# Performance work log

Hardware: AMD Instinct MI355X
Metric: run time of the kernel (lower is better)

The kernel has to match this reference:

```python
import jax, jax.numpy as jnp
import numpy as np

D_MODEL = 768
N_HEAD = 12
N_BR = 4
DH = D_MODEL // N_HEAD          # 64
H_TOT = N_BR * N_HEAD           # 48
K_TOP = 4
B, T = 2, 1024


def setup_inputs() -> dict:
    key = jax.random.key(0)
    ks = jax.random.split(key, 16)
    s = 0.02
    return {
        "A": jax.random.normal(ks[0], (B, T, D_MODEL), jnp.float32),
        "X": jax.random.normal(ks[1], (B, T, D_MODEL), jnp.float32),
        "WK_w": jax.random.normal(ks[2], (D_MODEL, D_MODEL), jnp.float32) * s,
        "WK_b": jax.random.normal(ks[3], (D_MODEL,), jnp.float32) * s,
        "WQ_w": jax.random.normal(ks[4], (D_MODEL * N_BR, D_MODEL), jnp.float32) * s,
        "wedge_A": jax.random.normal(ks[5], (DH, DH), jnp.float32) * s,
        "wedge_bias": jax.random.normal(ks[6], (H_TOT, DH), jnp.float32) * s,
        "sink": jax.random.normal(ks[7], (H_TOT,), jnp.float32) * s,
        "v_nulls": jax.random.normal(ks[8], (N_BR, D_MODEL), jnp.float32) * s,
        "V1_w": jax.random.normal(ks[9], (4 * DH, DH), jnp.float32) * s,
        "V1_b": jax.random.normal(ks[10], (4 * DH,), jnp.float32) * s,
        "V2_w": jax.random.normal(ks[11], (DH, 4 * DH), jnp.float32) * s,
        "V2_b": jax.random.normal(ks[12], (DH,), jnp.float32) * s,
        "WO_w": jax.random.normal(ks[13], (N_BR, D_MODEL, D_MODEL), jnp.float32) * s,
        "WO_b": jax.random.normal(ks[14], (N_BR, D_MODEL), jnp.float32) * s,
    }


def _wedge(x, wedge_A, wedge_bias):
    # S = (A - A^T) + diag_embed(id_bias); x: [B,H,T,Dh]
    skew = wedge_A - wedge_A.T                       # [Dh,Dh]
    S = skew[None, :, :] + jax.vmap(jnp.diag)(wedge_bias)  # [H,Dh,Dh]
    return x + jnp.einsum('bhtd,hde->bhte', x, S)


def _rope(x):
    # x: [B,H,T,Dh]; halves are interleaved-split then concatenated
    t_len = x.shape[2]
    inv_freq = 1.0 / (10000.0 ** (jnp.arange(0, DH, 2, dtype=jnp.float32) / DH))
    freqs = jnp.arange(t_len, dtype=jnp.float32)[:, None] * inv_freq[None, :]  # [T,Dh/2]
    cos = jnp.cos(freqs)[None, None]
    sin = jnp.sin(freqs)[None, None]
    x1 = x[..., 0::2]
    x2 = x[..., 1::2]
    return jnp.concatenate((-x2 * sin + x1 * cos, x1 * sin + x2 * cos), axis=-1)


def reference(A, X, WK_w, WK_b, WQ_w, wedge_A, wedge_bias, sink, v_nulls,
              V1_w, V1_b, V2_w, V2_b, WO_w, WO_b):
    b, t, c = A.shape
    scale = DH ** -0.5

    q = (A @ WQ_w.T).reshape(b, t, H_TOT, DH).transpose(0, 2, 1, 3)     # [B,Htot,T,Dh]
    k_base = X @ WK_w.T + WK_b
    k = k_base.reshape(b, t, N_HEAD, DH).transpose(0, 2, 1, 3)          # [B,Nsh,T,Dh]
    k = jnp.tile(k, (1, N_BR, 1, 1))                                    # [B,Htot,T,Dh]

    q = _rope(_wedge(q, wedge_A, wedge_bias))
    k = _rope(_wedge(k, wedge_A, wedge_bias))

    scores = jnp.einsum('bhtd,bhsd->bhts', q, k) * scale                # [B,Htot,T,T]
    causal = jnp.triu(jnp.ones((t, t), dtype=bool), k=1)
    scores = jnp.where(causal[None, None], -jnp.inf, scores)

    sinks = jnp.broadcast_to(sink.reshape(1, H_TOT, 1, 1), (b, H_TOT, t, 1))
    probs_full = jax.nn.softmax(jnp.concatenate([scores, sinks], axis=-1), axis=-1)
    probs_tokens = probs_full[..., :t]
    probs_sink = probs_full[..., t:]                                    # [B,Htot,T,1]

    k_top = min(K_TOP, t)
    vals, idxs = jax.lax.top_k(probs_tokens, k_top)                     # [B,Htot,T,K]
    weights = vals / (jnp.sum(vals, axis=-1, keepdims=True) + 1e-9)

    # gather top-k keys: [B,Htot,T,K,Dh]
    k_selected = jnp.take_along_axis(k[:, :, None, :, :], idxs[..., None], axis=3)
    marker = jnp.einsum('bhtk,bhtkd->bhtd', weights, k_selected)        # [B,Htot,T,Dh]

    h = jax.nn.gelu(marker @ V1_w.T + V1_b, approximate=False)
    out_tokens = h @ V2_w.T + V2_b                                      # [B,Htot,T,Dh]

    v_null = v_nulls.reshape(H_TOT, DH)[None, :, None, :]
    context = out_tokens + probs_sink * v_null                          # [B,Htot,T,Dh]

    context = context.reshape(b, N_BR, N_HEAD, t, DH)
    context = context.transpose(0, 1, 3, 2, 4).reshape(b, N_BR, t, c)   # [B,Nbr,T,C]

    y = jnp.einsum('bntc,ncd->bntd', context, WO_w) + WO_b[None, :, None, :]
    return y.mean(axis=1)
```

## Files before the change

kernel.cpp:

```cpp
#include <hip/hip_runtime.h>
#include <math.h>

constexpr int Bq  = 2;
constexpr int Tq  = 1024;
constexpr int HTq = 48;
constexpr float SCALE = 0.125f;

typedef __attribute__((ext_vector_type(8))) short short8;
typedef __attribute__((ext_vector_type(4))) float f32x4;

__device__ inline unsigned short f2bf(float x) {
    unsigned u = __float_as_uint(x);
    return (unsigned short)((u + 0x7FFF + ((u >> 16) & 1)) >> 16);
}

__device__ inline void split3(float x, unsigned short& p0, unsigned short& p1, unsigned short& p2) {
    p0 = f2bf(x);
    float f0 = __uint_as_float((unsigned)p0 << 16);
    float r0 = x - f0;
    p1 = f2bf(r0);
    float f1 = __uint_as_float((unsigned)p1 << 16);
    float r1 = r0 - f1;
    p2 = f2bf(r1);
}

__device__ inline float gelu_f(float x) {
    float z = 0.70710678118654752f * x;
    float az = fabsf(z);
    float t = __frcp_rn(1.0f + 0.3275911f * az);
    float poly = t * (0.254829592f + t * (-0.284496736f + t * (1.421413741f
               + t * (-1.453152027f + t * 1.061405429f))));
    float er = 1.0f - poly * __expf(-az * az);
    er = (z < 0.0f) ? -er : er;
    return 0.5f * x * (1.0f + er);
}

__global__ void trig_kernel(float* __restrict__ trig) {
    int i = blockIdx.x * 256 + threadIdx.x;
    int t = i >> 5, f = i & 31;
    float invf = powf(10000.0f, -(float)f * (1.0f / 32.0f));
    float ang = (float)t * invf;
    trig[i] = cosf(ang);
    trig[32768 + i] = sinf(ang);
}

__global__ __launch_bounds__(256) void fold_split_kernel(
    const float* __restrict__ Wsrc, const float* __restrict__ wA,
    const float* __restrict__ wbias, unsigned short* __restrict__ Wsp, int mode)
{
    const size_t WPL = (size_t)4608 * 768;
    __shared__ float sw[64][132];
    __shared__ float sk[64][65];
    int h = blockIdx.x, cb = blockIdx.y;
    int tid = threadIdx.x;
    const float* Wh = Wsrc + (size_t)h * 64 * 768 + cb * 128;
    for (int l = tid; l < 64 * 32; l += 256) {
        int d = l >> 5, c4 = l & 31;
        *(float4*)&sw[d][c4 * 4] = *(const float4*)(Wh + (size_t)d * 768 + c4 * 4);
    }
    for (int l = tid; l < 4096; l += 256) {
        int d = l >> 6, e = l & 63;
        sk[d][e] = wA[l] - wA[e * 64 + d];
    }
    __syncthreads();
    int tx = tid & 15, ty = tid >> 4;
    float acc4[4][8] = {};
    for (int d = 0; d < 64; d++) {
        float s0 = sk[d][ty * 4 + 0], s1 = sk[d][ty * 4 + 1];
        float s2 = sk[d][ty * 4 + 2], s3 = sk[d][ty * 4 + 3];
        float w_[8];
        *(float4*)&w_[0] = *(const float4*)&sw[d][tx * 8];
        *(float4*)&w_[4] = *(const float4*)&sw[d][tx * 8 + 4];
        #pragma unroll
        for (int j = 0; j < 8; j++) {
            acc4[0][j] += s0 * w_[j];
            acc4[1][j] += s1 * w_[j];
            acc4[2][j] += s2 * w_[j];
            acc4[3][j] += s3 * w_[j];
        }
    }
    #pragma unroll
    for (int i = 0; i < 4; i++) {
        int e = ty * 4 + i;
        float scale = (mode == 0) ? (1.0f + wbias[h * 64 + e]) : 1.0f;
        size_t row = (mode == 0) ? (size_t)(h * 64 + e) : (size_t)(3072 + h * 64 + e);
        #pragma unroll
        for (int j = 0; j < 8; j++) {
            int cl = tx * 8 + j;
            float wv = sw[e][cl] * scale + acc4[i][j];
            unsigned short p0, p1, p2;
            split3(wv, p0, p1, p2);
            size_t idx = row * 768 + cb * 128 + cl;
            Wsp[idx] = p0; Wsp[WPL + idx] = p1; Wsp[2 * WPL + idx] = p2;
        }
        if (mode == 1) {
            size_t row2 = (size_t)(3840 + h * 64 + e);
            #pragma unroll
            for (int j = 0; j < 8; j++) {
                int cl = tx * 8 + j;
                unsigned short p0, p1, p2;
                split3(sw[e][cl], p0, p1, p2);
                size_t idx = row2 * 768 + cb * 128 + cl;
                Wsp[idx] = p0; Wsp[WPL + idx] = p1; Wsp[2 * WPL + idx] = p2;
            }
        }
    }
}

__global__ void kbias_kernel(const float* __restrict__ WKb, const float* __restrict__ wA,
                             float* __restrict__ bcat) {
    int e = blockIdx.x * 256 + threadIdx.x;
    if (e < 768) {
        int hb = e >> 6, el = e & 63;
        float acc = 0.0f;
        for (int d = 0; d < 64; d++) {
            float sk = wA[d * 64 + el] - wA[el * 64 + d];
            acc += WKb[hb * 64 + d] * sk;
        }
        bcat[e] = WKb[e] + acc;
    } else if (e < 1536) {
        bcat[e] = WKb[e - 768];
    }
}

__global__ void split_act_kernel(const float* __restrict__ A, const float* __restrict__ X,
                                 unsigned short* __restrict__ Asp, unsigned short* __restrict__ Xsp)
{
    const size_t APL = (size_t)2048 * 768;
    int i = blockIdx.x * 256 + threadIdx.x;
    if (i >= 393216) return;
    float4 va = ((const float4*)A)[i];
    float4 vx = ((const float4*)X)[i];
    ushort4 a0, a1, a2, x0, x1, x2;
    split3(va.x, a0.x, a1.x, a2.x); split3(va.y, a0.y, a1.y, a2.y);
    split3(va.z, a0.z, a1.z, a2.z); split3(va.w, a0.w, a1.w, a2.w);
    split3(vx.x, x0.x, x1.x, x2.x); split3(vx.y, x0.y, x1.y, x2.y);
    split3(vx.z, x0.z, x1.z, x2.z); split3(vx.w, x0.w, x1.w, x2.w);
    ((ushort4*)(Asp))[i] = a0;
    ((ushort4*)(Asp + APL))[i] = a1;
    ((ushort4*)(Asp + 2 * APL))[i] = a2;
    ((ushort4*)(Xsp))[i] = x0;
    ((ushort4*)(Xsp + APL))[i] = x1;
    ((ushort4*)(Xsp + 2 * APL))[i] = x2;
}

__global__ __launch_bounds__(512) void proj_mfma_kernel(
    const unsigned short* __restrict__ Asp, const unsigned short* __restrict__ Xsp,
    const unsigned short* __restrict__ Wsp, const float* __restrict__ bcat,
    const float* __restrict__ trig, float* __restrict__ Qr, float* __restrict__ O2)
{
    const size_t APL = (size_t)2048 * 768;
    const size_t WPL = (size_t)4608 * 768;
    __shared__ unsigned short sA[3 * 128 * 40];
    __shared__ unsigned short sB[3 * 128 * 40];
    int bid = blockIdx.x;
    int swz = (bid & 7) * 72 + (bid >> 3);
    int nb = swz >> 4;
    int mb = swz & 15;
    bool isQ = (nb < 24);
    const unsigned short* Ab = isQ ? Asp : Xsp;
    int m0 = mb * 128, n0 = nb * 128;
    int tid = threadIdx.x;
    int w = tid >> 6, lane = tid & 63;
    int wm = w & 1, wn = w >> 1;
    int rf = lane & 15, kg = lane >> 4;
    int mbase = m0 + wm * 64;

    int sp_[3], sr_[3], ss_[3];
    #pragma unroll
    for (int i = 0; i < 3; i++) {
        int s = tid + i * 512;
        sp_[i] = s >> 9; sr_[i] = (s >> 2) & 127; ss_[i] = s & 3;
    }

    f32x4 acc[4][2] = {};
    for (int k0 = 0; k0 < 768; k0 += 32) {
        __syncthreads();
        #pragma unroll
        for (int i = 0; i < 3; i++) {
            short8 va = *(const short8*)(Ab + (size_t)sp_[i] * APL + (size_t)(m0 + sr_[i]) * 768 + k0 + ss_[i] * 8);
            short8 vb = *(const short8*)(Wsp + (size_t)sp_[i] * WPL + (size_t)(n0 + sr_[i]) * 768 + k0 + ss_[i] * 8);
            *(short8*)&sA[sp_[i] * 5120 + sr_[i] * 40 + ss_[i] * 8] = va;
            *(short8*)&sB[sp_[i] * 5120 + sr_[i] * 40 + ss_[i] * 8] = vb;
        }
        __syncthreads();

        short8 a0[4], a1[4], a2[4], b0[2], b1[2], b2[2];
        #pragma unroll
        for (int mi = 0; mi < 4; mi++) {
            int row = wm * 64 + mi * 16 + rf;
            a0[mi] = *(const short8*)&sA[0 * 5120 + row * 40 + kg * 8];
        }
        #pragma unroll
        for (int nj = 0; nj < 2; nj++) {
            int row = wn * 32 + nj * 16 + rf;
            b0[nj] = *(const short8*)&sB[0 * 5120 + row * 40 + kg * 8];
        }
        #pragma unroll
        for (int mi = 0; mi < 4; mi++)
            #pragma unroll
            for (int nj = 0; nj < 2; nj++)
                acc[mi][nj] = __builtin_amdgcn_mfma_f32_16x16x32_bf16(a0[mi], b0[nj], acc[mi][nj], 0, 0, 0);
        #pragma unroll
        for (int nj = 0; nj < 2; nj++) {
            int row = wn * 32 + nj * 16 + rf;
            b1[nj] = *(const short8*)&sB[1 * 5120 + row * 40 + kg * 8];
        }
        #pragma unroll
        for (int mi = 0; mi < 4; mi++)
            #pragma unroll
            for (int nj = 0; nj < 2; nj++)
                acc[mi][nj] = __builtin_amdgcn_mfma_f32_16x16x32_bf16(a0[mi], b1[nj], acc[mi][nj], 0, 0, 0);
        #pragma unroll
        for (int nj = 0; nj < 2; nj++) {
            int row = wn * 32 + nj * 16 + rf;
            b2[nj] = *(const short8*)&sB[2 * 5120 + row * 40 + kg * 8];
        }
        #pragma unroll
        for (int mi = 0; mi < 4; mi++)
            #pragma unroll
            for (int nj = 0; nj < 2; nj++)
                acc[mi][nj] = __builtin_amdgcn_mfma_f32_16x16x32_bf16(a0[mi], b2[nj], acc[mi][nj], 0, 0, 0);
        #pragma unroll
        for (int mi = 0; mi < 4; mi++) {
            int row = wm * 64 + mi * 16 + rf;
            a1[mi] = *(const short8*)&sA[1 * 5120 + row * 40 + kg * 8];
        }
        #pragma unroll
        for (int mi = 0; mi < 4; mi++)
            #pragma unroll
            for (int nj = 0; nj < 2; nj++)
                acc[mi][nj] = __builtin_amdgcn_mfma_f32_16x16x32_bf16(a1[mi], b0[nj], acc[mi][nj], 0, 0, 0);
        #pragma unroll
        for (int mi = 0; mi < 4; mi++)
            #pragma unroll
            for (int nj = 0; nj < 2; nj++)
                acc[mi][nj] = __builtin_amdgcn_mfma_f32_16x16x32_bf16(a1[mi], b1[nj], acc[mi][nj], 0, 0, 0);
        #pragma unroll
        for (int mi = 0; mi < 4; mi++) {
            int row = wm * 64 + mi * 16 + rf;
            a2[mi] = *(const short8*)&sA[2 * 5120 + row * 40 + kg * 8];
        }
        #pragma unroll
        for (int mi = 0; mi < 4; mi++)
            #pragma unroll
            for (int nj = 0; nj < 2; nj++)
                acc[mi][nj] = __builtin_amdgcn_mfma_f32_16x16x32_bf16(a2[mi], b0[nj], acc[mi][nj], 0, 0, 0);
    }

    if (isQ) {
        #pragma unroll
        for (int mi = 0; mi < 4; mi++) {
            #pragma unroll
            for (int r = 0; r < 4; r++) {
                int m = mbase + mi * 16 + kg * 4 + r;
                int b_ = m >> 10, t = m & 1023;
                #pragma unroll
                for (int nj = 0; nj < 2; nj++) {
                    int col_local = wn * 32 + nj * 16 + rf;
                    int h = nb * 2 + (col_local >> 6);
                    int d = col_local & 63;
                    int i = d >> 1;
                    float v = acc[mi][nj][r];
                    float pv = __shfl_xor(v, 1);
                    float c = trig[t * 32 + i];
                    float s = trig[32768 + t * 32 + i];
                    float outv = (rf & 1) ? (pv * s + v * c) : (v * c - pv * s);
                    int col = (rf & 1) ? (32 + i) : i;
                    size_t base = ((size_t)(b_ * 48 + h) * 1024 + t) * 64;
                    Qr[base + col] = outv;
                }
            }
        }
    } else {
        #pragma unroll
        for (int nj = 0; nj < 2; nj++) {
            int col = (n0 - 3072) + wn * 32 + nj * 16 + rf;
            float bv = bcat[col];
            #pragma unroll
            for (int mi = 0; mi < 4; mi++)
                #pragma unroll
                for (int r = 0; r < 4; r++) {
                    int m = mbase + mi * 16 + kg * 4 + r;
                    O2[(size_t)m * 1536 + col] = acc[mi][nj][r] + bv;
                }
        }
    }
}

__global__ void k_finish_kernel(const float* __restrict__ O2, const float* __restrict__ trig,
                                const float* __restrict__ wbias,
                                float* __restrict__ Kr, unsigned short* __restrict__ Kb16)
{
    int idx = blockIdx.x * 256 + threadIdx.x;
    int pr = idx & 31;
    int tmp = idx >> 5;
    int hb = tmp % 12;
    int bt = tmp / 12;
    int t = bt & 1023, b = bt >> 10;
    const float* yx = O2 + (size_t)bt * 1536 + hb * 64 + pr * 2;
    float y0 = yx[0], y1 = yx[1];
    float x0 = yx[768], x1 = yx[769];
    float cv = trig[t * 32 + pr], sv = trig[32768 + t * 32 + pr];
    #pragma unroll
    for (int r = 0; r < 4; r++) {
        int h = hb + 12 * r;
        float b0 = wbias[h * 64 + 2 * pr], b1 = wbias[h * 64 + 2 * pr + 1];
        float wz0 = y0 + x0 * b0;
        float wz1 = y1 + x1 * b1;
        float lo = wz0 * cv - wz1 * sv;
        float hi = wz0 * sv + wz1 * cv;
        size_t base = ((size_t)(b * 48 + h) * 1024 + t) * 64;
        Kr[base + pr] = lo;
        Kr[base + 32 + pr] = hi;
        Kb16[base + pr] = f2bf(lo);
        Kb16[base + 32 + pr] = f2bf(hi);
    }
}

__global__ __launch_bounds__(256) void attn_mfma_topk_kernel(
    const float* __restrict__ Qr, const float* __restrict__ Kr,
    const unsigned short* __restrict__ Kb, const float* __restrict__ sink,
    unsigned short* __restrict__ markerb, float* __restrict__ psink)
{
    const int bh = blockIdx.x;
    const int qb = 15 - (int)blockIdx.y;
    const int w = threadIdx.x >> 6, lane = threadIdx.x & 63;
    const int rf = lane & 15, kg = lane >> 4;
    const int h = bh % HTq;
    const int q0 = qb * 64 + w * 16;
    const size_t rowbase = (size_t)bh * Tq;

    short8 a0, a1;
    {
        const float* qp = Qr + (rowbase + q0 + rf) * 64 + kg * 8;
        float4 u0 = *(const float4*)qp;
        float4 u1 = *(const float4*)(qp + 4);
        float4 u2 = *(const float4*)(qp + 32);
        float4 u3 = *(const float4*)(qp + 36);
        a0[0]=(short)f2bf(u0.x); a0[1]=(short)f2bf(u0.y); a0[2]=(short)f2bf(u0.z); a0[3]=(short)f2bf(u0.w);
        a0[4]=(short)f2bf(u1.x); a0[5]=(short)f2bf(u1.y); a0[6]=(short)f2bf(u1.z); a0[7]=(short)f2bf(u1.w);
        a1[0]=(short)f2bf(u2.x); a1[1]=(short)f2bf(u2.y); a1[2]=(short)f2bf(u2.z); a1[3]=(short)f2bf(u2.w);
        a1[4]=(short)f2bf(u3.x); a1[5]=(short)f2bf(u3.y); a1[6]=(short)f2bf(u3.z); a1[7]=(short)f2bf(u3.w);
    }

    float m_[4], Z_[4], tv[4][4];
    int ti[4][4];
    #pragma unroll
    for (int r = 0; r < 4; r++) {
        m_[r] = -1e30f; Z_[r] = 0.0f;
        #pragma unroll
        for (int p = 0; p < 4; p++) { tv[r][p] = -INFINITY; ti[r][p] = -1; }
    }

    const int T = (q0 + 15) / 64 + 1;
    const unsigned short* Kbb = Kb + rowbase * 64;
    for (int tile = 0; tile < T; tile++) {
        const int s0 = tile << 6;
        f32x4 accs[4];
        #pragma unroll
        for (int kc = 0; kc < 4; kc++) {
            const unsigned short* kp = Kbb + (size_t)(s0 + kc * 16 + rf) * 64 + kg * 8;
            short8 b0 = *(const short8*)kp;
            short8 b1 = *(const short8*)(kp + 32);
            f32x4 acc = {0.f, 0.f, 0.f, 0.f};
            acc = __builtin_amdgcn_mfma_f32_16x16x32_bf16(a0, b0, acc, 0, 0, 0);
            acc = __builtin_amdgcn_mfma_f32_16x16x32_bf16(a1, b1, acc, 0, 0, 0);
            accs[kc] = acc;
        }
        const bool lastt = (tile == T - 1);
        #pragma unroll
        for (int r = 0; r < 4; r++) {
            const int trow = q0 + kg * 4 + r;
            float sv[4];
            #pragma unroll
            for (int kc = 0; kc < 4; kc++) {
                int k = s0 + kc * 16 + rf;
                float s = accs[kc][r] * SCALE;
                sv[kc] = (lastt && k > trow) ? -INFINITY : s;
            }
            float tm = fmaxf(fmaxf(sv[0], sv[1]), fmaxf(sv[2], sv[3]));
            float nm = fmaxf(m_[r], tm);
            float zz = Z_[r] * __expf(m_[r] - nm);
            #pragma unroll
            for (int kc = 0; kc < 4; kc++) zz += __expf(sv[kc] - nm);
            Z_[r] = zz; m_[r] = nm;
            #pragma unroll
            for (int kc = 0; kc < 4; kc++) {
                float v = sv[kc]; int id = s0 + kc * 16 + rf;
                #pragma unroll
                for (int p = 0; p < 4; p++) {
                    bool sw = v > tv[r][p];
                    float ov = tv[r][p]; int oi = ti[r][p];
                    tv[r][p] = sw ? v : ov;  ti[r][p] = sw ? id : oi;
                    v = sw ? ov : v;          id = sw ? oi : id;
                }
            }
        }
    }

    const float sk = sink[h];
    #pragma unroll 1
    for (int r = 0; r < 4; r++) {
        const int q = q0 + kg * 4 + r;
        float m = m_[r], Z = Z_[r];
        #pragma unroll
        for (int off = 1; off < 16; off <<= 1) {
            float om = __shfl_xor(m, off);
            float oz = __shfl_xor(Z, off);
            float nm = fmaxf(m, om);
            Z = Z * __expf(m - nm) + oz * __expf(om - nm);
            m = nm;
        }
        float av[4]; int ai[4];
        #pragma unroll
        for (int p = 0; p < 4; p++) { av[p] = tv[r][p]; ai[p] = ti[r][p]; }
        float cvv[8]; int ci[8];
        #pragma unroll
        for (int rd = 0; rd < 8; rd++) {
            float v = av[0]; int id = ai[0];
            #pragma unroll
            for (int off = 1; off < 16; off <<= 1) {
                float ov = __shfl_xor(v, off);
                int oi = __shfl_xor(id, off);
                bool take = (ov > v) || ((ov == v) && ((unsigned)oi < (unsigned)id));
                v = take ? ov : v; id = take ? oi : id;
            }
            cvv[rd] = v; ci[rd] = id;
            bool own = (ai[0] == id) && (av[0] == v);
            av[0] = own ? av[1] : av[0];  ai[0] = own ? ai[1] : ai[0];
            av[1] = own ? av[2] : av[1];  ai[1] = own ? ai[2] : ai[1];
            av[2] = own ? av[3] : av[2];  ai[2] = own ? ai[3] : ai[2];
            av[3] = own ? -INFINITY : av[3]; ai[3] = own ? -1 : ai[3];
        }
        const float4 qv = *(const float4*)(Qr + (rowbase + q) * 64 + rf * 4);
        float sc[8];
        #pragma unroll
        for (int c = 0; c < 8; c++) {
            int idx = ci[c] < 0 ? 0 : ci[c];
            const float4 kv = *(const float4*)(Kr + (rowbase + idx) * 64 + rf * 4);
            float p = qv.x * kv.x + qv.y * kv.y + qv.z * kv.z + qv.w * kv.w;
            #pragma unroll
            for (int off = 1; off < 16; off <<= 1) p += __shfl_xor(p, off);
            sc[c] = (ci[c] < 0) ? -1e30f : p * SCALE;
        }
        float bv[4]; int bi[4];
        #pragma unroll
        for (int rd = 0; rd < 4; rd++) {
            float v = sc[0]; int id = ci[0];
            #pragma unroll
            for (int c = 1; c < 8; c++) {
                bool take = (sc[c] > v) || ((sc[c] == v) && ((unsigned)ci[c] < (unsigned)id));
                v = take ? sc[c] : v; id = take ? ci[c] : id;
            }
            bv[rd] = v; bi[rd] = id;
            #pragma unroll
            for (int c = 0; c < 8; c++) {
                bool kill = (ci[c] == id) && (sc[c] == v);
                sc[c] = kill ? -3e30f : sc[c];
            }
        }
        float mf = fmaxf(m, sk);
        float Zf = Z * __expf(m - mf) + __expf(sk - mf);
        float e0 = __expf(bv[0] - mf), e1 = __expf(bv[1] - mf);
        float e2 = __expf(bv[2] - mf), e3 = __expf(bv[3] - mf);
        float wsum = e0 + e1 + e2 + e3 + Zf * 1e-9f;
        float w0 = e0 / wsum, w1 = e1 / wsum, w2 = e2 / wsum, w3 = e3 / wsum;
        int i0 = bi[0] < 0 ? 0 : bi[0];
        int i1 = bi[1] < 0 ? 0 : bi[1];
        int i2 = bi[2] < 0 ? 0 : bi[2];
        int i3 = bi[3] < 0 ? 0 : bi[3];
        const float4 k0 = *(const float4*)(Kr + (rowbase + i0) * 64 + rf * 4);
        const float4 k1 = *(const float4*)(Kr + (rowbase + i1) * 64 + rf * 4);
        const float4 k2 = *(const float4*)(Kr + (rowbase + i2) * 64 + rf * 4);
        const float4 k3 = *(const float4*)(Kr + (rowbase + i3) * 64 + rf * 4);
        float mx = w0 * k0.x + w1 * k1.x + w2 * k2.x + w3 * k3.x;
        float my = w0 * k0.y + w1 * k1.y + w2 * k2.y + w3 * k3.y;
        float mz = w0 * k0.z + w1 * k1.z + w2 * k2.z + w3 * k3.z;
        float mw = w0 * k0.w + w1 * k1.w + w2 * k2.w + w3 * k3.w;
        ushort4 mo;
        mo.x = f2bf(mx); mo.y = f2bf(my); mo.z = f2bf(mz); mo.w = f2bf(mw);
        *(ushort4*)(markerb + (rowbase + q) * 64 + rf * 4) = mo;
        if (rf == 0) psink[rowbase + q] = __expf(sk - mf) / Zf;
    }
}

__global__ void cvt_bf16_kernel(const float* __restrict__ in,
                                unsigned short* __restrict__ out, int n4)
{
    int i = blockIdx.x * 256 + threadIdx.x;
    if (i < n4) {
        float4 v = ((const float4*)in)[i];
        ushort4 o;
        o.x = f2bf(v.x); o.y = f2bf(v.y); o.z = f2bf(v.z); o.w = f2bf(v.w);
        ((ushort4*)out)[i] = o;
    }
}

__global__ __launch_bounds__(256) void wo_transpose_kernel(
    const float* __restrict__ WOw, unsigned short* __restrict__ WOt)
{
    __shared__ float tl[64][65];
    int tid = threadIdx.x;
    int n = blockIdx.z;
    int c0 = blockIdx.x * 64, d0 = blockIdx.y * 64;
    const float* src = WOw + (size_t)n * 768 * 768;
    for (int l = tid; l < 64 * 16; l += 256) {
        int r = l >> 4, q = l & 15;
        float4 v = *(const float4*)(src + (size_t)(c0 + r) * 768 + d0 + q * 4);
        tl[r][q * 4 + 0] = v.x; tl[r][q * 4 + 1] = v.y;
        tl[r][q * 4 + 2] = v.z; tl[r][q * 4 + 3] = v.w;
    }
    __syncthreads();
    for (int l = tid; l < 64 * 16; l += 256) {
        int d = l >> 4, q = l & 15;
        ushort4 o;
        o.x = f2bf(tl[q * 4 + 0][d]); o.y = f2bf(tl[q * 4 + 1][d]);
        o.z = f2bf(tl[q * 4 + 2][d]); o.w = f2bf(tl[q * 4 + 3][d]);
        *(ushort4*)(WOt + (size_t)n * 768 * 768 + (size_t)(d0 + d) * 768 + c0 + q * 4) = o;
    }
}

__global__ __launch_bounds__(256) void mlp_mfma_kernel(
    const unsigned short* __restrict__ markerb, const float* __restrict__ psink,
    const unsigned short* __restrict__ V1b16, const float* __restrict__ V1bias,
    const unsigned short* __restrict__ V2b16, const float* __restrict__ V2bias,
    const float* __restrict__ vnulls, unsigned short* __restrict__ ctxb)
{
    __shared__ float h_lds[4][16][65];
    int tid = threadIdx.x;
    int w = tid >> 6, lane = tid & 63;
    int rf = lane & 15, kg = lane >> 4;
    size_t r0 = (size_t)blockIdx.x * 64 + 16 * w;

    short8 a1[2];
    #pragma unroll
    for (int kk = 0; kk < 2; kk++)
        a1[kk] = *(const short8*)(markerb + (r0 + rf) * 64 + kk * 32 + kg * 8);

    f32x4 acc2[4] = {};
    for (int ch = 0; ch < 4; ch++) {
        f32x4 acc1[4] = {};
        #pragma unroll
        for (int nj = 0; nj < 4; nj++)
            #pragma unroll
            for (int kk = 0; kk < 2; kk++) {
                short8 b1 = *(const short8*)(V1b16 + (size_t)(ch * 64 + nj * 16 + rf) * 64 + kk * 32 + kg * 8);
                acc1[nj] = __builtin_amdgcn_mfma_f32_16x16x32_bf16(a1[kk], b1, acc1[nj], 0, 0, 0);
            }
        __syncthreads();
        #pragma unroll
        for (int nj = 0; nj < 4; nj++) {
            float bb = V1bias[ch * 64 + nj * 16 + rf];
            #pragma unroll
            for (int r = 0; r < 4; r++) {
                float x = acc1[nj][r] + bb;
                h_lds[w][kg * 4 + r][nj * 16 + rf] = gelu_f(x);
            }
        }
        __syncthreads();
        #pragma unroll
        for (int kk = 0; kk < 2; kk++) {
            const float* hp = &h_lds[w][rf][kk * 32 + kg * 8];
            float4 p0 = *(const float4*)hp;
            float4 p1 = *(const float4*)(hp + 4);
            short8 a2;
            a2[0] = (short)f2bf(p0.x); a2[1] = (short)f2bf(p0.y);
            a2[2] = (short)f2bf(p0.z); a2[3] = (short)f2bf(p0.w);
            a2[4] = (short)f2bf(p1.x); a2[5] = (short)f2bf(p1.y);
            a2[6] = (short)f2bf(p1.z); a2[7] = (short)f2bf(p1.w);
            #pragma unroll
            for (int njo = 0; njo < 4; njo++) {
                short8 b2 = *(const short8*)(V2b16 + (size_t)(njo * 16 + rf) * 256 + ch * 64 + kk * 32 + kg * 8);
                acc2[njo] = __builtin_amdgcn_mfma_f32_16x16x32_bf16(a2, b2, acc2[njo], 0, 0, 0);
            }
        }
    }
    #pragma unroll
    for (int r = 0; r < 4; r++) {
        size_t R = r0 + kg * 4 + r;
        int bh = (int)(R >> 10), t = (int)(R & 1023);
        int b = bh / 48, h = bh % 48;
        int n = h / 12, head = h % 12;
        float ps = psink[R];
        size_t base = ((size_t)((b * 4 + n) * 1024 + t)) * 768 + head * 64;
        #pragma unroll
        for (int njo = 0; njo < 4; njo++) {
            int d = njo * 16 + rf;
            float v = acc2[njo][r] + V2bias[d] + ps * vnulls[h * 64 + d];
            ctxb[base + d] = f2bf(v);
        }
    }
}

__global__ __launch_bounds__(256) void gemm_wo_mfma(
    const unsigned short* __restrict__ ctxb, const unsigned short* __restrict__ WOtb,
    const float* __restrict__ WOb, float* __restrict__ Out)
{
    __shared__ unsigned short sA[64 * 64];
    __shared__ unsigned short sB[64 * 64];
    int tid = threadIdx.x;
    int w = tid >> 6, lane = tid & 63;
    int wm = w >> 1, wn = w & 1;
    int rf = lane & 15, kg = lane >> 4;
    int m0 = blockIdx.x * 64, n0 = blockIdx.y * 64;
    int b = m0 >> 10, t0 = m0 & 1023;
    int c0 = tid * 2, c1 = tid * 2 + 1;
    int ra = c0 >> 3, ca = c0 & 7, rb = c1 >> 3, cb = c1 & 7;
    f32x4 acc[2][2] = {};
    for (int n = 0; n < 4; n++) {
        const unsigned short* Ab = ctxb + ((size_t)((b * 4 + n) * 1024 + t0)) * 768;
        const unsigned short* Bb = WOtb + (size_t)n * 768 * 768 + (size_t)n0 * 768;
        for (int k0 = 0; k0 < 768; k0 += 64) {
            __syncthreads();
            *(short8*)&sA[ra * 64 + ((ca ^ (ra & 7)) * 8)] = *(const short8*)(Ab + (size_t)ra * 768 + k0 + ca * 8);
            *(short8*)&sA[rb * 64 + ((cb ^ (rb & 7)) * 8)] = *(const short8*)(Ab + (size_t)rb * 768 + k0 + cb * 8);
            *(short8*)&sB[ra * 64 + ((ca ^ (ra & 7)) * 8)] = *(const short8*)(Bb + (size_t)ra * 768 + k0 + ca * 8);
            *(short8*)&sB[rb * 64 + ((cb ^ (rb & 7)) * 8)] = *(const short8*)(Bb + (size_t)rb * 768 + k0 + cb * 8);
            __syncthreads();
            #pragma unroll
            for (int kk = 0; kk < 2; kk++) {
                int kc = kk * 4 + kg;
                int rA0 = wm * 32 + rf, rA1 = wm * 32 + 16 + rf;
                int rB0 = wn * 32 + rf, rB1 = wn * 32 + 16 + rf;
                short8 a0v = *(const short8*)&sA[rA0 * 64 + ((kc ^ (rA0 & 7)) * 8)];
                short8 a1v = *(const short8*)&sA[rA1 * 64 + ((kc ^ (rA1 & 7)) * 8)];
                short8 b0v = *(const short8*)&sB[rB0 * 64 + ((kc ^ (rB0 & 7)) * 8)];
                short8 b1v = *(const short8*)&sB[rB1 * 64 + ((kc ^ (rB1 & 7)) * 8)];
                acc[0][0] = __builtin_amdgcn_mfma_f32_16x16x32_bf16(a0v, b0v, acc[0][0], 0, 0, 0);
                acc[0][1] = __builtin_amdgcn_mfma_f32_16x16x32_bf16(a0v, b1v, acc[0][1], 0, 0, 0);
                acc[1][0] = __builtin_amdgcn_mfma_f32_16x16x32_bf16(a1v, b0v, acc[1][0], 0, 0, 0);
                acc[1][1] = __builtin_amdgcn_mfma_f32_16x16x32_bf16(a1v, b1v, acc[1][1], 0, 0, 0);
            }
        }
    }
    #pragma unroll
    for (int nj = 0; nj < 2; nj++) {
        int col = n0 + wn * 32 + nj * 16 + rf;
        float bm = WOb[col] + WOb[768 + col] + WOb[1536 + col] + WOb[2304 + col];
        #pragma unroll
        for (int mi = 0; mi < 2; mi++)
            #pragma unroll
            for (int r = 0; r < 4; r++) {
                int row = m0 + wm * 32 + mi * 16 + kg * 4 + r;
                Out[(size_t)row * 768 + col] = 0.25f * (acc[mi][nj][r] + bm);
            }
    }
}

extern "C" void kernel_launch(void* const* d_in, const int* in_sizes, int n_in,
                              void* d_out, int out_size, void* d_ws, size_t ws_size,
                              hipStream_t stream) {
    const float* A      = (const float*)d_in[0];
    const float* X      = (const float*)d_in[1];
    const float* WKw    = (const float*)d_in[2];
    const float* WKb    = (const float*)d_in[3];
    const float* WQw    = (const float*)d_in[4];
    const float* wA     = (const float*)d_in[5];
    const float* wB     = (const float*)d_in[6];
    const float* sink   = (const float*)d_in[7];
    const float* vnulls = (const float*)d_in[8];
    const float* V1w    = (const float*)d_in[9];
    const float* V1b    = (const float*)d_in[10];
    const float* V2w    = (const float*)d_in[11];
    const float* V2b    = (const float*)d_in[12];
    const float* WOw    = (const float*)d_in[13];
    const float* WOb    = (const float*)d_in[14];
    float* out = (float*)d_out;
    (void)in_sizes; (void)n_in; (void)out_size; (void)ws_size;

    float* ws = (float*)d_ws;
    size_t off = 0;
    float* Qr   = ws + off;  off += 6291456;
    float* Kr   = ws + off;  off += 6291456;
    float* trig = ws + off;  off += 65536;
    float* bcat = ws + off;  off += 2048;
    float* O2   = ws + off;  off += 3145728;
    float* Wsp_f = ws + off; off += 5308416;
    unsigned short* Wsp = (unsigned short*)Wsp_f;
    unsigned short* Asp = (unsigned short*)(ws + off); off += 2359296;
    unsigned short* Xsp = (unsigned short*)(ws + off); off += 2359296;
    unsigned short* markerb = (unsigned short*)O2;
    unsigned short* Kb16 = Wsp;
    float* psink = Wsp_f + 3145728;
    unsigned short* V1b16 = Xsp;
    unsigned short* V2b16 = V1b16 + 16384;
    unsigned short* WOtb  = Asp;
    unsigned short* ctxb  = (unsigned short*)Qr;

    trig_kernel<<<128, 256, 0, stream>>>(trig);
    fold_split_kernel<<<dim3(48, 6), 256, 0, stream>>>(WQw, wA, wB, Wsp, 0);
    fold_split_kernel<<<dim3(12, 6), 256, 0, stream>>>(WKw, wA, wB, Wsp, 1);
    kbias_kernel<<<6, 256, 0, stream>>>(WKb, wA, bcat);
    split_act_kernel<<<1536, 256, 0, stream>>>(A, X, Asp, Xsp);
    proj_mfma_kernel<<<576, 512, 0, stream>>>(Asp, Xsp, Wsp, bcat, trig, Qr, O2);
    k_finish_kernel<<<3072, 256, 0, stream>>>(O2, trig, wB, Kr, Kb16);
    attn_mfma_topk_kernel<<<dim3(96, 16), 256, 0, stream>>>(Qr, Kr, Kb16, sink, markerb, psink);
    cvt_bf16_kernel<<<16, 256, 0, stream>>>(V1w, V1b16, 4096);
    cvt_bf16_kernel<<<16, 256, 0, stream>>>(V2w, V2b16, 4096);
    wo_transpose_kernel<<<dim3(12, 12, 4), 256, 0, stream>>>(WOw, WOtb);
    mlp_mfma_kernel<<<1536, 256, 0, stream>>>(markerb, psink, V1b16, V1b, V2b16, V2b, vnulls, ctxb);
    gemm_wo_mfma<<<dim3(32, 12), 256, 0, stream>>>(ctxb, WOtb, WOb, out);
}
```

Before: 362.7 us.

## Pair causal query blocks, prefetch K tiles, and pack top-k keys into uints

Each attention block now handles two query blocks (qb and 15-qb) so every block does the same amount of causal work, and the grid is halved. The K tile loop is double-buffered in registers so the next tile's loads are issued before the current tile's softmax and top-k work, and the causal mask is applied only on the final diagonal tile. The per-lane top-4 now holds one packed unsigned key (order-preserving score bits with the index in the low 10 bits), which makes the insertion and cross-lane reductions cheaper. Dropping the low mantissa bits can change candidate order on near-ties, but candidates are rescored exactly in fp32 afterwards; the extra prefetch buffers raise register pressure.

```diff
diff --git a/kernel.cpp b/kernel.cpp
--- a/kernel.cpp
+++ b/kernel.cpp
@@ -324,164 +324,228 @@
     unsigned short* __restrict__ markerb, float* __restrict__ psink)
 {
     const int bh = blockIdx.x;
-    const int qb = 15 - (int)blockIdx.y;
+    const int y  = blockIdx.y;
     const int w = threadIdx.x >> 6, lane = threadIdx.x & 63;
     const int rf = lane & 15, kg = lane >> 4;
     const int h = bh % HTq;
-    const int q0 = qb * 64 + w * 16;
     const size_t rowbase = (size_t)bh * Tq;
-
-    short8 a0, a1;
-    {
-        const float* qp = Qr + (rowbase + q0 + rf) * 64 + kg * 8;
-        float4 u0 = *(const float4*)qp;
-        float4 u1 = *(const float4*)(qp + 4);
-        float4 u2 = *(const float4*)(qp + 32);
-        float4 u3 = *(const float4*)(qp + 36);
-        a0[0]=(short)f2bf(u0.x); a0[1]=(short)f2bf(u0.y); a0[2]=(short)f2bf(u0.z); a0[3]=(short)f2bf(u0.w);
-        a0[4]=(short)f2bf(u1.x); a0[5]=(short)f2bf(u1.y); a0[6]=(short)f2bf(u1.z); a0[7]=(short)f2bf(u1.w);
-        a1[0]=(short)f2bf(u2.x); a1[1]=(short)f2bf(u2.y); a1[2]=(short)f2bf(u2.z); a1[3]=(short)f2bf(u2.w);
-        a1[4]=(short)f2bf(u3.x); a1[5]=(short)f2bf(u3.y); a1[6]=(short)f2bf(u3.z); a1[7]=(short)f2bf(u3.w);
-    }
-
-    float m_[4], Z_[4], tv[4][4];
-    int ti[4][4];
-    #pragma unroll
-    for (int r = 0; r < 4; r++) {
-        m_[r] = -1e30f; Z_[r] = 0.0f;
-        #pragma unroll
-        for (int p = 0; p < 4; p++) { tv[r][p] = -INFINITY; ti[r][p] = -1; }
-    }
-
-    const int T = (q0 + 15) / 64 + 1;
     const unsigned short* Kbb = Kb + rowbase * 64;
-    for (int tile = 0; tile < T; tile++) {
-        const int s0 = tile << 6;
-        f32x4 accs[4];
-        #pragma unroll
-        for (int kc = 0; kc < 4; kc++) {
-            const unsigned short* kp = Kbb + (size_t)(s0 + kc * 16 + rf) * 64 + kg * 8;
-            short8 b0 = *(const short8*)kp;
-            short8 b1 = *(const short8*)(kp + 32);
-            f32x4 acc = {0.f, 0.f, 0.f, 0.f};
-            acc = __builtin_amdgcn_mfma_f32_16x16x32_bf16(a0, b0, acc, 0, 0, 0);
-            acc = __builtin_amdgcn_mfma_f32_16x16x32_bf16(a1, b1, acc, 0, 0, 0);
-            accs[kc] = acc;
-        }
-        const bool lastt = (tile == T - 1);
+    const float sk = sink[h];
+
+    #pragma unroll 1
+    for (int g = 0; g < 2; g++) {
+        const int qb = g ? y : 15 - y;
+        const int q0 = qb * 64 + w * 16;
+
+        short8 a0, a1;
+        {
+            const float* qp = Qr + (rowbase + q0 + rf) * 64 + kg * 8;
+            float4 u0 = *(const float4*)qp;
+            float4 u1 = *(const float4*)(qp + 4);
+            float4 u2 = *(const float4*)(qp + 32);
+            float4 u3 = *(const float4*)(qp + 36);
+            a0[0]=(short)f2bf(u0.x); a0[1]=(short)f2bf(u0.y); a0[2]=(short)f2bf(u0.z); a0[3]=(short)f2bf(u0.w);
+            a0[4]=(short)f2bf(u1.x); a0[5]=(short)f2bf(u1.y); a0[6]=(short)f2bf(u1.z); a0[7]=(short)f2bf(u1.w);
+            a1[0]=(short)f2bf(u2.x); a1[1]=(short)f2bf(u2.y); a1[2]=(short)f2bf(u2.z); a1[3]=(short)f2bf(u2.w);
+            a1[4]=(short)f2bf(u3.x); a1[5]=(short)f2bf(u3.y); a1[6]=(short)f2bf(u3.z); a1[7]=(short)f2bf(u3.w);
+        }
+
+        float m_[4], Z_[4];
+        unsigned t_[4][4];
         #pragma unroll
         for (int r = 0; r < 4; r++) {
-            const int trow = q0 + kg * 4 + r;
-            float sv[4];
+            m_[r] = -1e30f; Z_[r] = 0.0f;
+            t_[r][0] = 0u; t_[r][1] = 0u; t_[r][2] = 0u; t_[r][3] = 0u;
+        }
+
+        short8 cA0[4], cA1[4], cB0[4], cB1[4];
+        {
+            const unsigned short* p = Kbb + (size_t)rf * 64 + kg * 8;
             #pragma unroll
             for (int kc = 0; kc < 4; kc++) {
-                int k = s0 + kc * 16 + rf;
-                float s = accs[kc][r] * SCALE;
-                sv[kc] = (lastt && k > trow) ? -INFINITY : s;
-            }
-            float tm = fmaxf(fmaxf(sv[0], sv[1]), fmaxf(sv[2], sv[3]));
-            float nm = fmaxf(m_[r], tm);
-            float zz = Z_[r] * __expf(m_[r] - nm);
-            #pragma unroll
-            for (int kc = 0; kc < 4; kc++) zz += __expf(sv[kc] - nm);
-            Z_[r] = zz; m_[r] = nm;
+                cA0[kc] = *(const short8*)(p + kc * 1024);
+                cA1[kc] = *(const short8*)(p + kc * 1024 + 32);
+            }
+        }
+
+        auto body = [&](short8 (&cb0)[4], short8 (&cb1)[4],
+                        short8 (&nb0)[4], short8 (&nb1)[4], int tile) {
+            f32x4 accs[4];
             #pragma unroll
             for (int kc = 0; kc < 4; kc++) {
-                float v = sv[kc]; int id = s0 + kc * 16 + rf;
-                #pragma unroll
-                for (int p = 0; p < 4; p++) {
-                    bool sw = v > tv[r][p];
-                    float ov = tv[r][p]; int oi = ti[r][p];
-                    tv[r][p] = sw ? v : ov;  ti[r][p] = sw ? id : oi;
-                    v = sw ? ov : v;          id = sw ? oi : id;
+                f32x4 acc = {0.f, 0.f, 0.f, 0.f};
+                acc = __builtin_amdgcn_mfma_f32_16x16x32_bf16(a0, cb0[kc], acc, 0, 0, 0);
+                acc = __builtin_amdgcn_mfma_f32_16x16x32_bf16(a1, cb1[kc], acc, 0, 0, 0);
+                accs[kc] = acc;
+            }
+            const unsigned short* np = Kbb + (size_t)((tile + 1) * 64 + rf) * 64 + kg * 8;
+            #pragma unroll
+            for (int kc = 0; kc < 4; kc++) {
+                nb0[kc] = *(const short8*)(np + kc * 1024);
+                nb1[kc] = *(const short8*)(np + kc * 1024 + 32);
+            }
+            const int s0 = tile << 6;
+            #pragma unroll
+            for (int r = 0; r < 4; r++) {
+                float sv[4];
+                #pragma unroll
+                for (int kc = 0; kc < 4; kc++) sv[kc] = accs[kc][r] * SCALE;
+                #pragma unroll
+                for (int kc = 0; kc < 4; kc++) {
+                    unsigned u = __float_as_uint(sv[kc]);
+                    unsigned key = u ^ ((unsigned)(((int)u) >> 31) | 0x80000000u);
+                    unsigned c = (key & 0xFFFFFC00u) | (unsigned)(s0 + kc * 16 + rf);
+                    unsigned n;
+                    n = t_[r][0] > c ? t_[r][0] : c;  c = t_[r][0] > c ? c : t_[r][0];  t_[r][0] = n;
+                    n = t_[r][1] > c ? t_[r][1] : c;  c = t_[r][1] > c ? c : t_[r][1];  t_[r][1] = n;
+                    n = t_[r][2] > c ? t_[r][2] : c;  c = t_[r][2] > c ? c : t_[r][2];  t_[r][2] = n;
+                    t_[r][3] = t_[r][3] > c ? t_[r][3] : c;
                 }
-            }
-        }
-    }
-
-    const float sk = sink[h];
-    #pragma unroll 1
-    for (int r = 0; r < 4; r++) {
-        const int q = q0 + kg * 4 + r;
-        float m = m_[r], Z = Z_[r];
-        #pragma unroll
-        for (int off = 1; off < 16; off <<= 1) {
-            float om = __shfl_xor(m, off);
-            float oz = __shfl_xor(Z, off);
-            float nm = fmaxf(m, om);
-            Z = Z * __expf(m - nm) + oz * __expf(om - nm);
-            m = nm;
-        }
-        float av[4]; int ai[4];
-        #pragma unroll
-        for (int p = 0; p < 4; p++) { av[p] = tv[r][p]; ai[p] = ti[r][p]; }
-        float cvv[8]; int ci[8];
-        #pragma unroll
-        for (int rd = 0; rd < 8; rd++) {
-            float v = av[0]; int id = ai[0];
+                float tm = fmaxf(fmaxf(sv[0], sv[1]), fmaxf(sv[2], sv[3]));
+                float nm = fmaxf(m_[r], tm);
+                float zz = Z_[r] * __expf(m_[r] - nm);
+                #pragma unroll
+                for (int kc = 0; kc < 4; kc++) zz += __expf(sv[kc] - nm);
+                Z_[r] = zz; m_[r] = nm;
+            }
+        };
+
+        int tile = 0;
+        for (; tile + 1 < qb; tile += 2) {
+            body(cA0, cA1, cB0, cB1, tile);
+            body(cB0, cB1, cA0, cA1, tile + 1);
+        }
+        if (tile < qb) {
+            body(cA0, cA1, cB0, cB1, tile);
+            #pragma unroll
+            for (int kc = 0; kc < 4; kc++) { cA0[kc] = cB0[kc]; cA1[kc] = cB1[kc]; }
+        }
+
+        {
+            f32x4 accs[4];
+            #pragma unroll
+            for (int kc = 0; kc < 4; kc++) {
+                f32x4 acc = {0.f, 0.f, 0.f, 0.f};
+                acc = __builtin_amdgcn_mfma_f32_16x16x32_bf16(a0, cA0[kc], acc, 0, 0, 0);
+                acc = __builtin_amdgcn_mfma_f32_16x16x32_bf16(a1, cA1[kc], acc, 0, 0, 0);
+                accs[kc] = acc;
+            }
+            const int s0 = qb << 6;
+            #pragma unroll
+            for (int r = 0; r < 4; r++) {
+                const int trow = q0 + kg * 4 + r;
+                float sv[4];
+                unsigned pk[4];
+                #pragma unroll
+                for (int kc = 0; kc < 4; kc++) {
+                    int k = s0 + kc * 16 + rf;
+                    bool ok = (k <= trow);
+                    float s = accs[kc][r] * SCALE;
+                    sv[kc] = ok ? s : -INFINITY;
+                    unsigned u = __float_as_uint(s);
+                    unsigned key = u ^ ((unsigned)(((int)u) >> 31) | 0x80000000u);
+                    unsigned c = (key & 0xFFFFFC00u) | (unsigned)k;
+                    pk[kc] = ok ? c : 0u;
+                }
+                #pragma unroll
+                for (int kc = 0; kc < 4; kc++) {
+                    unsigned c = pk[kc], n;
+                    n = t_[r][0] > c ? t_[r][0] : c;  c = t_[r][0] > c ? c : t_[r][0];  t_[r][0] = n;
+                    n = t_[r][1] > c ? t_[r][1] : c;  c = t_[r][1] > c ? c : t_[r][1];  t_[r][1] = n;
+                    n = t_[r][2] > c ? t_[r][2] : c;  c = t_[r][2] > c ? c : t_[r][2];  t_[r][2] = n;
+                    t_[r][3] = t_[r][3] > c ? t_[r][3] : c;
+                }
+                float tm = fmaxf(fmaxf(sv[0], sv[1]), fmaxf(sv[2], sv[3]));
+                float nm = fmaxf(m_[r], tm);
+                float zz = Z_[r] * __expf(m_[r] - nm);
+                #pragma unroll
+                for (int kc = 0; kc < 4; kc++) zz += __expf(sv[kc] - nm);
+                Z_[r] = zz; m_[r] = nm;
+            }
+        }
+
+        #pragma unroll 1
+        for (int r = 0; r < 4; r++) {
+            const int q = q0 + kg * 4 + r;
+            float m = m_[r], Z = Z_[r];
             #pragma unroll
             for (int off = 1; off < 16; off <<= 1) {
-                float ov = __shfl_xor(v, off);
-                int oi = __shfl_xor(id, off);
-                bool take = (ov > v) || ((ov == v) && ((unsigned)oi < (unsigned)id));
-                v = take ? ov : v; id = take ? oi : id;
-            }
-            cvv[rd] = v; ci[rd] = id;
-            bool own = (ai[0] == id) && (av[0] == v);
-            av[0] = own ? av[1] : av[0];  ai[0] = own ? ai[1] : ai[0];
-            av[1] = own ? av[2] : av[1];  ai[1] = own ? ai[2] : ai[1];
-            av[2] = own ? av[3] : av[2];  ai[2] = own ? ai[3] : ai[2];
-            av[3] = own ? -INFINITY : av[3]; ai[3] = own ? -1 : ai[3];
-        }
-        const float4 qv = *(const float4*)(Qr + (rowbase + q) * 64 + rf * 4);
-        float sc[8];
-        #pragma unroll
-        for (int c = 0; c < 8; c++) {
-            int idx = ci[c] < 0 ? 0 : ci[c];
-            const float4 kv = *(const float4*)(Kr + (rowbase + idx) * 64 + rf * 4);
-            float p = qv.x * kv.x + qv.y * kv.y + qv.z * kv.z + qv.w * kv.w;
-            #pragma unroll
-            for (int off = 1; off < 16; off <<= 1) p += __shfl_xor(p, off);
-            sc[c] = (ci[c] < 0) ? -1e30f : p * SCALE;
-        }
-        float bv[4]; int bi[4];
-        #pragma unroll
-        for (int rd = 0; rd < 4; rd++) {
-            float v = sc[0]; int id = ci[0];
-            #pragma unroll
-            for (int c = 1; c < 8; c++) {
-                bool take = (sc[c] > v) || ((sc[c] == v) && ((unsigned)ci[c] < (unsigned)id));
-                v = take ? sc[c] : v; id = take ? ci[c] : id;
-            }
-            bv[rd] = v; bi[rd] = id;
+                float om = __shfl_xor(m, off);
+                float oz = __shfl_xor(Z, off);
+                float nm = fmaxf(m, om);
+                Z = Z * __expf(m - nm) + oz * __expf(om - nm);
+                m = nm;
+            }
+            unsigned l0 = t_[r][0], l1 = t_[r][1], l2 = t_[r][2], l3 = t_[r][3];
+            unsigned ck[8];
+            #pragma unroll
+            for (int rd = 0; rd < 8; rd++) {
+                unsigned v = l0;
+                #pragma unroll
+                for (int off = 1; off < 16; off <<= 1) {
+                    unsigned ov = (unsigned)__shfl_xor((int)v, off);
+                    v = v > ov ? v : ov;
+                }
+                ck[rd] = v;
+                bool own = (l0 == v);
+                l0 = own ? l1 : l0;
+                l1 = own ? l2 : l1;
+                l2 = own ? l3 : l2;
+                l3 = own ? 0u : l3;
+            }
+            const float4 qv = *(const float4*)(Qr + (rowbase + q) * 64 + rf * 4);
+            float sc[8]; int ci[8];
             #pragma unroll
             for (int c = 0; c < 8; c++) {
-                bool kill = (ci[c] == id) && (sc[c] == v);
-                sc[c] = kill ? -3e30f : sc[c];
-            }
-        }
-        float mf = fmaxf(m, sk);
-        float Zf = Z * __expf(m - mf) + __expf(sk - mf);
-        float e0 = __expf(bv[0] - mf), e1 = __expf(bv[1] - mf);
-        float e2 = __expf(bv[2] - mf), e3 = __expf(bv[3] - mf);
-        float wsum = e0 + e1 + e2 + e3 + Zf * 1e-9f;
-        float w0 = e0 / wsum, w1 = e1 / wsum, w2 = e2 / wsum, w3 = e3 / wsum;
-        int i0 = bi[0] < 0 ? 0 : bi[0];
-        int i1 = bi[1] < 0 ? 0 : bi[1];
-        int i2 = bi[2] < 0 ? 0 : bi[2];
-        int i3 = bi[3] < 0 ? 0 : bi[3];
-        const float4 k0 = *(const float4*)(Kr + (rowbase + i0) * 64 + rf * 4);
-        const float4 k1 = *(const float4*)(Kr + (rowbase + i1) * 64 + rf * 4);
-        const float4 k2 = *(const float4*)(Kr + (rowbase + i2) * 64 + rf * 4);
-        const float4 k3 = *(const float4*)(Kr + (rowbase + i3) * 64 + rf * 4);
-        float mx = w0 * k0.x + w1 * k1.x + w2 * k2.x + w3 * k3.x;
-        float my = w0 * k0.y + w1 * k1.y + w2 * k2.y + w3 * k3.y;
-        float mz = w0 * k0.z + w1 * k1.z + w2 * k2.z + w3 * k3.z;
-        float mw = w0 * k0.w + w1 * k1.w + w2 * k2.w + w3 * k3.w;
-        ushort4 mo;
-        mo.x = f2bf(mx); mo.y = f2bf(my); mo.z = f2bf(mz); mo.w = f2bf(mw);
-        *(ushort4*)(markerb + (rowbase + q) * 64 + rf * 4) = mo;
-        if (rf == 0) psink[rowbase + q] = __expf(sk - mf) / Zf;
+                bool valid = (ck[c] != 0u);
+                int idx = (int)(ck[c] & 1023u);
+                int lidx = valid ? idx : 0;
+                const float4 kv = *(const float4*)(Kr + (rowbase + lidx) * 64 + rf * 4);
+                float p = qv.x * kv.x + qv.y * kv.y + qv.z * kv.z + qv.w * kv.w;
+                #pragma unroll
+                for (int off = 1; off < 16; off <<= 1) p += __shfl_xor(p, off);
+                sc[c] = valid ? p * SCALE : -1e30f;
+                ci[c] = valid ? idx : -1;
+            }
+            float bv[4]; int bi[4];
+            #pragma unroll
+            for (int rd = 0; rd < 4; rd++) {
+                float v = sc[0]; int id = ci[0];
+                #pragma unroll
+                for (int c = 1; c < 8; c++) {
+                    bool take = (sc[c] > v) || ((sc[c] == v) && ((unsigned)ci[c] < (unsigned)id));
+                    v = take ? sc[c] : v; id = take ? ci[c] : id;
+                }
+                bv[rd] = v; bi[rd] = id;
+                #pragma unroll
+                for (int c = 0; c < 8; c++) {
+                    bool kill = (ci[c] == id) && (sc[c] == v);
+                    sc[c] = kill ? -3e30f : sc[c];
+                }
+            }
+            float mf = fmaxf(m, sk);
+            float Zf = Z * __expf(m - mf) + __expf(sk - mf);
+            float e0 = __expf(bv[0] - mf), e1 = __expf(bv[1] - mf);
+            float e2 = __expf(bv[2] - mf), e3 = __expf(bv[3] - mf);
+            float wsum = e0 + e1 + e2 + e3 + Zf * 1e-9f;
+            float w0 = e0 / wsum, w1 = e1 / wsum, w2 = e2 / wsum, w3 = e3 / wsum;
+            int i0 = bi[0] < 0 ? 0 : bi[0];
+            int i1 = bi[1] < 0 ? 0 : bi[1];
+            int i2 = bi[2] < 0 ? 0 : bi[2];
+            int i3 = bi[3] < 0 ? 0 : bi[3];
+            const float4 k0 = *(const float4*)(Kr + (rowbase + i0) * 64 + rf * 4);
+            const float4 k1 = *(const float4*)(Kr + (rowbase + i1) * 64 + rf * 4);
+            const float4 k2 = *(const float4*)(Kr + (rowbase + i2) * 64 + rf * 4);
+            const float4 k3 = *(const float4*)(Kr + (rowbase + i3) * 64 + rf * 4);
+            float mx = w0 * k0.x + w1 * k1.x + w2 * k2.x + w3 * k3.x;
+            float my = w0 * k0.y + w1 * k1.y + w2 * k2.y + w3 * k3.y;
+            float mz = w0 * k0.z + w1 * k1.z + w2 * k2.z + w3 * k3.z;
+            float mw = w0 * k0.w + w1 * k1.w + w2 * k2.w + w3 * k3.w;
+            ushort4 mo;
+            mo.x = f2bf(mx); mo.y = f2bf(my); mo.z = f2bf(mz); mo.w = f2bf(mw);
+            *(ushort4*)(markerb + (rowbase + q) * 64 + rf * 4) = mo;
+            if (rf == 0) psink[rowbase + q] = __expf(sk - mf) / Zf;
+        }
     }
 }
 
@@ -695,7 +759,7 @@
     split_act_kernel<<<1536, 256, 0, stream>>>(A, X, Asp, Xsp);
     proj_mfma_kernel<<<576, 512, 0, stream>>>(Asp, Xsp, Wsp, bcat, trig, Qr, O2);
     k_finish_kernel<<<3072, 256, 0, stream>>>(O2, trig, wB, Kr, Kb16);
-    attn_mfma_topk_kernel<<<dim3(96, 16), 256, 0, stream>>>(Qr, Kr, Kb16, sink, markerb, psink);
+    attn_mfma_topk_kernel<<<dim3(96, 8), 256, 0, stream>>>(Qr, Kr, Kb16, sink, markerb, psink);
     cvt_bf16_kernel<<<16, 256, 0, stream>>>(V1w, V1b16, 4096);
     cvt_bf16_kernel<<<16, 256, 0, stream>>>(V2w, V2b16, 4096);
     wo_transpose_kernel<<<dim3(12, 12, 4), 256, 0, stream>>>(WOw, WOtb);
```

Result: faster. 353.6 us (median of 2 runs) (-2.5%).
